# Optimization experiments

Hardware: AMD Instinct MI355X
Metric: run time of the kernel (lower is better)

## Reference

```python
import jax, jax.numpy as jnp
import numpy as np

H, D = 16, 64            # total_num_heads, head_dim
E = H * D                # embed_dim = 1024
NUM_BUCKETS, MAX_DIST = 32, 128
SCALING = D ** -0.5


def _rel_buckets(seq_len):
    # WavLM bidirectional relative position buckets (static, computed in numpy)
    ctx = np.arange(seq_len)[:, None]
    mem = np.arange(seq_len)[None, :]
    rel = mem - ctx                                  # [s, s]
    nb = NUM_BUCKETS // 2
    buckets = (rel > 0).astype(np.int64) * nb
    rp = np.abs(rel)
    max_exact = nb // 2
    is_small = rp < max_exact
    large = max_exact + (
        np.log(np.maximum(rp, 1) / max_exact) / np.log(MAX_DIST / max_exact) * (nb - max_exact)
    ).astype(np.int64)
    large = np.minimum(large, nb - 1)
    buckets = buckets + np.where(is_small, rp, large)
    return jnp.asarray(buckets)


def setup_inputs() -> dict:
    key = jax.random.key(0)
    ks = jax.random.split(key, 12)
    s = 0.02
    x = jax.random.normal(ks[0], (8, 1024, E), jnp.float32)
    Wq = jax.random.normal(ks[1], (E, H * D), jnp.float32) * s
    bq = jnp.zeros((H * D,), jnp.float32)
    Wk = jax.random.normal(ks[2], (E, H * D), jnp.float32) * s
    bk = jnp.zeros((H * D,), jnp.float32)
    Wv = jax.random.normal(ks[3], (E, H * D), jnp.float32) * s
    bv = jnp.zeros((H * D,), jnp.float32)
    Wo = jax.random.normal(ks[4], (H * D, E), jnp.float32) * s
    bo = jnp.zeros((E,), jnp.float32)
    rel_embed = jax.random.normal(ks[5], (NUM_BUCKETS, H), jnp.float32) * s
    gru_w = jax.random.normal(ks[6], (D, 8), jnp.float32) * s
    gru_b = jnp.zeros((8,), jnp.float32)
    gru_const = jnp.ones((1, H, 1, 1), jnp.float32)
    return {"x": x, "Wq": Wq, "bq": bq, "Wk": Wk, "bk": bk, "Wv": Wv, "bv": bv,
            "Wo": Wo, "bo": bo, "rel_embed": rel_embed,
            "gru_w": gru_w, "gru_b": gru_b, "gru_const": gru_const}


def reference(x, Wq, bq, Wk, bk, Wv, bv, Wo, bo, rel_embed, gru_w, gru_b, gru_const):
    b, s, e = x.shape
    # relative position bias: [H, s, s]
    buckets = _rel_buckets(s)
    pos_bias = jnp.transpose(rel_embed[buckets], (2, 0, 1))
    # gated relative position (gru_rel_pos)
    qlayer = x.reshape(b, s, H, D).transpose(0, 2, 1, 3)            # [b,H,s,D]
    g = jnp.einsum('bhsd,de->bhse', qlayer, gru_w) + gru_b          # [b,H,s,8]
    g = jax.nn.sigmoid(g.reshape(b, H, s, 2, 4).sum(-1))           # [b,H,s,2]
    gate_a, gate_b = g[..., :1], g[..., 1:]                         # [b,H,s,1]
    gate = gate_a * (gate_b * gru_const - 1.0) + 2.0                # [b,H,s,1]
    bias = gate * pos_bias[None]                                    # [b,H,s,s]
    # projections -> [b,H,s,D]
    q = (x @ Wq + bq).reshape(b, s, H, D).transpose(0, 2, 1, 3)
    k = (x @ Wk + bk).reshape(b, s, H, D).transpose(0, 2, 1, 3)
    v = (x @ Wv + bv).reshape(b, s, H, D).transpose(0, 2, 1, 3)
    scores = SCALING * jnp.einsum('bhqd,bhkd->bhqk', q, k) + bias
    w = jax.nn.softmax(scores, axis=-1)   # includes stable max-subtract
    out = jnp.einsum('bhqk,bhkd->bhqd', w, v)
    out = out.transpose(0, 2, 1, 3).reshape(b, s, H * D)
    return out @ Wo + bo
```

## Files before the change

kernel.cpp:

```cpp
#include <hip/hip_runtime.h>
#include <hip/hip_bf16.h>
#include <math.h>


typedef __attribute__((ext_vector_type(8))) short short8;
typedef __attribute__((ext_vector_type(4))) float f32x4;

#define LDSP(p) ((__attribute__((address_space(3))) void*)(p))
#define GLBP(p) ((const __attribute__((address_space(1))) void*)(p))

__device__ __forceinline__ void async_ld16(const void* src, void* dst) {
  __builtin_amdgcn_global_load_lds(GLBP(src), LDSP(dst), 16, 0, 0);
}
__device__ __forceinline__ unsigned short f2bf(float f) {
  __hip_bfloat16 h = __float2bfloat16(f);
  return __builtin_bit_cast(unsigned short, h);
}
#if __has_builtin(__builtin_amdgcn_exp2f)
#define EXP2(x) __builtin_amdgcn_exp2f(x)
#else
#define EXP2(x) exp2f(x)
#endif

__global__ __launch_bounds__(256) void prep_all(
    const float* __restrict__ x, const float* __restrict__ gw,
    const float* __restrict__ gb, const float* __restrict__ gcst,
    const float* __restrict__ W0, const float* __restrict__ W1,
    const float* __restrict__ W2, const float* __restrict__ W3,
    const float* __restrict__ rel_embed,
    unsigned short* __restrict__ xb, float* __restrict__ gate_ws,
    unsigned short* __restrict__ Wt_all, float* __restrict__ btab) {
  __shared__ __align__(16) float tile[64][68];
  const int bid = blockIdx.x, t = threadIdx.x;
  if (bid < 8192) {
    float* xr = &tile[0][0];
    const float4 v = *(const float4*)&x[(size_t)bid * 1024 + t * 4];
    *(float4*)&xr[t * 4] = v;
    ushort4 o;
    o.x = f2bf(v.x); o.y = f2bf(v.y); o.z = f2bf(v.z); o.w = f2bf(v.w);
    *(ushort4*)&xb[(size_t)bid * 1024 + t * 4] = o;
    __syncthreads();
    const int h = t >> 4, i = t & 15;
    float pa = 0.f, pb = 0.f;
    #pragma unroll
    for (int j = 0; j < 4; ++j) {
      const int d = i * 4 + j;
      const float xv = xr[h * 64 + d];
      const float* wr = &gw[d * 8];
      pa += xv * (wr[0] + wr[1] + wr[2] + wr[3]);
      pb += xv * (wr[4] + wr[5] + wr[6] + wr[7]);
    }
    #pragma unroll
    for (int msk = 1; msk <= 8; msk <<= 1) {
      pa += __shfl_xor(pa, msk);
      pb += __shfl_xor(pb, msk);
    }
    if (i == 0) {
      const float ba = gb[0] + gb[1] + gb[2] + gb[3];
      const float bb = gb[4] + gb[5] + gb[6] + gb[7];
      const float ga  = 1.f / (1.f + __expf(-(pa + ba)));
      const float gbv = 1.f / (1.f + __expf(-(pb + bb)));
      const float gv  = ga * (gbv * gcst[h] - 1.f) + 2.f;
      const int b = bid >> 10, s = bid & 1023;
      gate_ws[(b * 16 + h) * 1024 + s] = gv;
    }
  } else if (bid < 9216) {
    const int zz = bid - 8192;
    const int z = zz >> 8;
    const float* W = (z == 0) ? W0 : (z == 1) ? W1 : (z == 2) ? W2 : W3;
    unsigned short* Wt = Wt_all + (size_t)z * 1048576;
    const int n0 = (zz & 15) * 64, k0 = ((zz >> 4) & 15) * 64;
    const int c = (t & 15) * 4, r = t >> 4;
    #pragma unroll
    for (int i = 0; i < 4; ++i)
      *(float4*)&tile[r + i * 16][c] =
          *(const float4*)&W[(size_t)(k0 + r + i * 16) * 1024 + n0 + c];
    __syncthreads();
    #pragma unroll
    for (int i = 0; i < 4; ++i) {
      const int n = r + i * 16;
      ushort4 o;
      o.x = f2bf(tile[c + 0][n]); o.y = f2bf(tile[c + 1][n]);
      o.z = f2bf(tile[c + 2][n]); o.w = f2bf(tile[c + 3][n]);
      *(ushort4*)&Wt[(size_t)(n0 + n) * 1024 + k0 + c] = o;
    }
  } else {
    const int idx = (bid - 9216) * 256 + t;
    if (idx < 2047) {
      const int rel = idx - 1023;
      int bucket = (rel > 0) ? 16 : 0;
      const int rp = rel < 0 ? -rel : rel;
      if (rp < 8) {
        bucket += rp;
      } else {
        const double lv = log((double)rp / 8.0) / log(16.0) * 8.0;
        int large = 8 + (int)lv;
        bucket += (large < 15) ? large : 15;
      }
      #pragma unroll
      for (int h = 0; h < 16; ++h)
        btab[h * 2048 + idx] = rel_embed[bucket * 16 + h];
    }
  }
}

template <int SWAP>
__device__ __forceinline__ void gemm_core(
    const unsigned short* __restrict__ A, const unsigned short* __restrict__ Bt,
    unsigned short* As, unsigned short* Bs, const int m0, const int n0,
    f32x4 acc[4][4]) {
  const int t = threadIdx.x, w = t >> 6, l = t & 63;
  const int lr = l & 15, lg = l >> 4;
  const int wr = w >> 1, wc = w & 1;

  const unsigned short* asrc[4];
  const unsigned short* bsrc[4];
  unsigned short* adst[4];
  unsigned short* bdst[4];
  #pragma unroll
  for (int i = 0; i < 4; ++i) {
    const int p = (w * 4 + i) * 64 + l, r = p >> 3, c = p & 7;
    const int cs = c ^ (r & 7);
    asrc[i] = A + (size_t)(m0 + r) * 1024 + cs * 8;
    bsrc[i] = Bt + (size_t)(n0 + r) * 1024 + cs * 8;
    adst[i] = &As[(w * 4 + i) * 512];
    bdst[i] = &Bs[(w * 4 + i) * 512];
  }

  int offA[2][4], offB[2][4];
  #pragma unroll
  for (int ks = 0; ks < 2; ++ks)
    #pragma unroll
    for (int mt = 0; mt < 4; ++mt) {
      offA[ks][mt] = (wr * 64 + mt * 16 + lr) * 64 + ((ks * 4 + lg) ^ (lr & 7)) * 8;
      offB[ks][mt] = (wc * 64 + mt * 16 + lr) * 64 + ((ks * 4 + lg) ^ (lr & 7)) * 8;
    }

  for (int k0 = 0; k0 < 16; ++k0) {
    #pragma unroll
    for (int i = 0; i < 4; ++i) {
      async_ld16(asrc[i], adst[i]);
      async_ld16(bsrc[i], bdst[i]);
      asrc[i] += 64;
      bsrc[i] += 64;
    }
    __syncthreads();
    #pragma unroll
    for (int ks = 0; ks < 2; ++ks) {
      short8 af[4], bf[4];
      #pragma unroll
      for (int mt = 0; mt < 4; ++mt) af[mt] = *(const short8*)&As[offA[ks][mt]];
      #pragma unroll
      for (int nt = 0; nt < 4; ++nt) bf[nt] = *(const short8*)&Bs[offB[ks][nt]];
      #pragma unroll
      for (int mt = 0; mt < 4; ++mt)
        #pragma unroll
        for (int nt = 0; nt < 4; ++nt)
          acc[mt][nt] = SWAP
              ? __builtin_amdgcn_mfma_f32_16x16x32_bf16(bf[nt], af[mt], acc[mt][nt], 0, 0, 0)
              : __builtin_amdgcn_mfma_f32_16x16x32_bf16(af[mt], bf[nt], acc[mt][nt], 0, 0, 0);
    }
    __syncthreads();
  }
}

__global__ __launch_bounds__(256) void gemm_qkv(
    const unsigned short* __restrict__ A, const unsigned short* __restrict__ wt_all,
    const float* __restrict__ bq, const float* __restrict__ bk,
    const float* __restrict__ bv, unsigned short* __restrict__ q_ws,
    unsigned short* __restrict__ k_ws, unsigned short* __restrict__ vt_ws) {
  __shared__ __align__(16) unsigned short As[128 * 64];
  __shared__ __align__(16) unsigned short Bs[128 * 64];
  const int which = blockIdx.y >> 3;
  const int m0 = blockIdx.x * 128, n0 = (blockIdx.y & 7) * 128;
  const unsigned short* Bt = wt_all + (size_t)which * 1048576;

  const int t = threadIdx.x, w = t >> 6, l = t & 63;
  const int lr = l & 15, lg = l >> 4;
  const int wr = w >> 1, wc = w & 1;
  const int mbase = m0 + wr * 64, nbase = n0 + wc * 64;

  f32x4 acc[4][4];
  #pragma unroll
  for (int mt = 0; mt < 4; ++mt)
    #pragma unroll
    for (int nt = 0; nt < 4; ++nt) acc[mt][nt] = (f32x4){0.f, 0.f, 0.f, 0.f};

  if (which == 2) {
    gemm_core<0>(A, Bt, As, Bs, m0, n0, acc);
    #pragma unroll
    for (int mt = 0; mt < 4; ++mt) {
      const int m4 = mbase + mt * 16 + lg * 4;
      const int b = m4 >> 10, s = m4 & 1023;
      #pragma unroll
      for (int nt = 0; nt < 4; ++nt) {
        const int n = nbase + nt * 16 + lr, h = n >> 6, d = n & 63;
        const float bvv = bv[n];
        ushort4 o;
        o.x = f2bf(acc[mt][nt][0] + bvv);
        o.y = f2bf(acc[mt][nt][1] + bvv);
        o.z = f2bf(acc[mt][nt][2] + bvv);
        o.w = f2bf(acc[mt][nt][3] + bvv);
        *(ushort4*)&vt_ws[(size_t)(b * 16 + h) * 65536 + (size_t)d * 1024 + s] = o;
      }
    }
  } else {
    gemm_core<1>(A, Bt, As, Bs, m0, n0, acc);
    unsigned short* dst = (which == 0) ? q_ws : k_ws;
    const float* bias = (which == 0) ? bq : bk;
    const float scale = (which == 0) ? 0.18033688011f : 1.0f;
    #pragma unroll
    for (int nt = 0; nt < 4; ++nt) {
      const int n4 = nbase + nt * 16 + lg * 4;
      const int h = n4 >> 6, d = n4 & 63;
      const float4 b4 = *(const float4*)&bias[n4];
      #pragma unroll
      for (int mt = 0; mt < 4; ++mt) {
        const int m = mbase + mt * 16 + lr;
        const int b = m >> 10, s = m & 1023;
        ushort4 o;
        o.x = f2bf((acc[mt][nt][0] + b4.x) * scale);
        o.y = f2bf((acc[mt][nt][1] + b4.y) * scale);
        o.z = f2bf((acc[mt][nt][2] + b4.z) * scale);
        o.w = f2bf((acc[mt][nt][3] + b4.w) * scale);
        *(ushort4*)&dst[(size_t)(b * 16 + h) * 65536 + s * 64 + d] = o;
      }
    }
  }
}

__global__ __launch_bounds__(256) void gemm_out(
    const unsigned short* __restrict__ A, const unsigned short* __restrict__ Bt,
    const float* __restrict__ bias, float* __restrict__ C) {
  __shared__ __align__(16) unsigned short As[128 * 64];
  __shared__ __align__(16) unsigned short Bs[128 * 64];
  const int m0 = blockIdx.x * 128, n0 = blockIdx.y * 128;
  f32x4 acc[4][4];
  #pragma unroll
  for (int mt = 0; mt < 4; ++mt)
    #pragma unroll
    for (int nt = 0; nt < 4; ++nt) acc[mt][nt] = (f32x4){0.f, 0.f, 0.f, 0.f};
  gemm_core<1>(A, Bt, As, Bs, m0, n0, acc);

  const int t = threadIdx.x, w = t >> 6, l = t & 63;
  const int lr = l & 15, lg = l >> 4;
  const int wr = w >> 1, wc = w & 1;
  const int mbase = m0 + wr * 64, nbase = n0 + wc * 64;
  #pragma unroll
  for (int nt = 0; nt < 4; ++nt) {
    const int n4 = nbase + nt * 16 + lg * 4;
    const float4 b4 = *(const float4*)&bias[n4];
    #pragma unroll
    for (int mt = 0; mt < 4; ++mt) {
      const int m = mbase + mt * 16 + lr;
      float4 o;
      o.x = acc[mt][nt][0] + b4.x;
      o.y = acc[mt][nt][1] + b4.y;
      o.z = acc[mt][nt][2] + b4.z;
      o.w = acc[mt][nt][3] + b4.w;
      *(float4*)&C[(size_t)m * 1024 + n4] = o;
    }
  }
}

__global__ __launch_bounds__(512) void attn_mfma(
    const unsigned short* __restrict__ q_ws, const unsigned short* __restrict__ k_ws,
    const unsigned short* __restrict__ vt_ws, const float* __restrict__ gate_ws,
    const float* __restrict__ btab, unsigned short* __restrict__ ctx) {
  __shared__ __align__(16) unsigned short Ks[2][64 * 64];
  __shared__ __align__(16) unsigned short Vts[64 * 64];
  __shared__ __align__(16) unsigned short Ps[8 * 1024];
  __shared__ __align__(16) float biasl[1216];
  __shared__ float gates[128];
  __shared__ float scl[128];

  const int t = threadIdx.x, w = t >> 6, l = t & 63;
  const int lr = l & 15, lg = l >> 4;
  const int bh = blockIdx.x, h = bh & 15, b = bh >> 4;
  const int q0 = blockIdx.y * 128;
  const size_t hb = (size_t)bh * 65536;

  short8 qf[2];
  #pragma unroll
  for (int ks = 0; ks < 2; ++ks)
    qf[ks] = *(const short8*)(q_ws + hb + (size_t)(q0 + w * 16 + lr) * 64 +
                              (ks * 4 + lg) * 8);

  {
    const int p = t, r = p >> 3, c = p & 7;
    const int cs = c ^ (r & 7);
    async_ld16(k_ws + hb + (size_t)r * 64 + cs * 8, &Ks[0][w * 512]);
  }
  {
    const float* bt = btab + h * 2048 + (896 - q0);
    const int u = t * 4;
    if (u < 1216) *(float4*)&biasl[u] = *(const float4*)&bt[u];
  }
  if (t < 128) gates[t] = gate_ws[bh * 1024 + q0 + t];
  asm volatile("s_waitcnt vmcnt(0) lgkmcnt(0)" ::: "memory");
  __builtin_amdgcn_s_barrier();
  __builtin_amdgcn_sched_barrier(0);

  int pwoff[4], proff[2], offF[2][4];
  #pragma unroll
  for (int nt = 0; nt < 4; ++nt)
    pwoff[nt] = w * 2048 + ((lr * 128 + nt * 32 + lg * 8) ^ ((lr & 7) << 4));
  #pragma unroll
  for (int ks = 0; ks < 2; ++ks) {
    proff[ks] = w * 2048 + ((lr * 128 + ks * 64 + lg * 16) ^ ((lr & 7) << 4));
    #pragma unroll
    for (int nt = 0; nt < 4; ++nt)
      offF[ks][nt] = (nt * 16 + lr) * 64 + ((ks * 4 + lg) ^ (lr & 7)) * 8;
  }

  float mcur = -1e30f, lsum = 0.f;
  f32x4 acc_o[4];
  #pragma unroll
  for (int dt = 0; dt < 4; ++dt) acc_o[dt] = (f32x4){0.f, 0.f, 0.f, 0.f};
  const float gtl = gates[w * 16 + lr] * 1.44269504f;
  const int ub = 127 - w * 16 - lr;
  char* Pb = (char*)Ps;

  int pcur = 0;
  for (int kt = 0; kt < 16; ++kt) {
    {
      const int p = t, r = p >> 3, c = p & 7;
      const int cs = c ^ (r & 7);
      async_ld16(vt_ws + hb + (size_t)r * 1024 + kt * 64 + cs * 8, &Vts[w * 512]);
      if (kt < 15)
        async_ld16(k_ws + hb + (size_t)(kt + 1) * 4096 + (size_t)r * 64 + cs * 8,
                   &Ks[pcur ^ 1][w * 512]);
    }

    const int bb = kt * 64 + ub + lg * 4;
    f32x4 accs[4];
    #pragma unroll
    for (int nt = 0; nt < 4; ++nt) {
      accs[nt][0] = gtl * biasl[bb + nt * 16 + 0];
      accs[nt][1] = gtl * biasl[bb + nt * 16 + 1];
      accs[nt][2] = gtl * biasl[bb + nt * 16 + 2];
      accs[nt][3] = gtl * biasl[bb + nt * 16 + 3];
    }

    __builtin_amdgcn_s_setprio(1);
    #pragma unroll
    for (int ks = 0; ks < 2; ++ks) {
      #pragma unroll
      for (int nt = 0; nt < 4; ++nt) {
        const short8 kf = *(const short8*)&Ks[pcur][offF[ks][nt]];
        accs[nt] = __builtin_amdgcn_mfma_f32_16x16x32_bf16(kf, qf[ks], accs[nt], 0, 0, 0);
      }
    }
    __builtin_amdgcn_s_setprio(0);

    float tm = -1e30f;
    #pragma unroll
    for (int nt = 0; nt < 4; ++nt)
      tm = fmaxf(fmaxf(tm, fmaxf(accs[nt][0], accs[nt][1])),
                 fmaxf(accs[nt][2], accs[nt][3]));
    tm = fmaxf(tm, __shfl_xor(tm, 16));
    tm = fmaxf(tm, __shfl_xor(tm, 32));

    const int skip = __all(tm <= mcur + 11.5f);
    float sc = 1.0f;
    if (!skip) {
      const float mn = fmaxf(mcur, tm);
      sc = EXP2(mcur - mn);
      mcur = mn;
      if (lg == 0) scl[w * 16 + lr] = sc;
    }

    float ps = 0.f;
    #pragma unroll
    for (int nt = 0; nt < 4; ++nt) {
      const float p0 = EXP2(accs[nt][0] - mcur);
      const float p1 = EXP2(accs[nt][1] - mcur);
      const float p2 = EXP2(accs[nt][2] - mcur);
      const float p3 = EXP2(accs[nt][3] - mcur);
      ps += (p0 + p1) + (p2 + p3);
      short4 pk;
      pk.x = (short)f2bf(p0); pk.y = (short)f2bf(p1);
      pk.z = (short)f2bf(p2); pk.w = (short)f2bf(p3);
      *(short4*)(Pb + pwoff[nt]) = pk;
    }
    lsum = skip ? (lsum + ps) : (lsum * sc + ps);

    if (kt < 15) {
      asm volatile("s_waitcnt vmcnt(1) lgkmcnt(0)" ::: "memory");
    } else {
      asm volatile("s_waitcnt vmcnt(0) lgkmcnt(0)" ::: "memory");
    }
    __builtin_amdgcn_s_barrier();
    __builtin_amdgcn_sched_barrier(0);

    if (!skip) {
      const float s0 = scl[w * 16 + lg * 4 + 0];
      const float s1 = scl[w * 16 + lg * 4 + 1];
      const float s2 = scl[w * 16 + lg * 4 + 2];
      const float s3 = scl[w * 16 + lg * 4 + 3];
      #pragma unroll
      for (int dt = 0; dt < 4; ++dt) {
        acc_o[dt][0] *= s0; acc_o[dt][1] *= s1;
        acc_o[dt][2] *= s2; acc_o[dt][3] *= s3;
      }
    }

    __builtin_amdgcn_s_setprio(1);
    #pragma unroll
    for (int ks = 0; ks < 2; ++ks) {
      const short8 pf = *(const short8*)(Pb + proff[ks]);
      #pragma unroll
      for (int dt = 0; dt < 4; ++dt) {
        const short8 vf = *(const short8*)&Vts[offF[ks][dt]];
        acc_o[dt] = __builtin_amdgcn_mfma_f32_16x16x32_bf16(pf, vf, acc_o[dt], 0, 0, 0);
      }
    }
    __builtin_amdgcn_s_setprio(0);

    asm volatile("s_waitcnt vmcnt(0)" ::: "memory");
    __builtin_amdgcn_s_barrier();
    __builtin_amdgcn_sched_barrier(0);
    pcur ^= 1;
  }

  lsum += __shfl_xor(lsum, 16);
  lsum += __shfl_xor(lsum, 32);
  if (lg == 0) scl[w * 16 + lr] = 1.0f / lsum;
  asm volatile("s_waitcnt lgkmcnt(0)" ::: "memory");
  __builtin_amdgcn_s_barrier();
  float inv[4];
  #pragma unroll
  for (int i = 0; i < 4; ++i) inv[i] = scl[w * 16 + lg * 4 + i];
  #pragma unroll
  for (int i = 0; i < 4; ++i) {
    const int q = q0 + w * 16 + lg * 4 + i;
    const size_t rowoff = ((size_t)(b * 1024 + q) * 16 + h) * 64;
    #pragma unroll
    for (int dt = 0; dt < 4; ++dt)
      ctx[rowoff + dt * 16 + lr] = f2bf(acc_o[dt][i] * inv[i]);
  }
}

extern "C" void kernel_launch(void* const* d_in, const int* in_sizes, int n_in,
                              void* d_out, int out_size, void* d_ws, size_t ws_size,
                              hipStream_t stream) {
  const float* x    = (const float*)d_in[0];
  const float* Wq   = (const float*)d_in[1];
  const float* bq   = (const float*)d_in[2];
  const float* Wk   = (const float*)d_in[3];
  const float* bk   = (const float*)d_in[4];
  const float* Wv   = (const float*)d_in[5];
  const float* bv   = (const float*)d_in[6];
  const float* Wo   = (const float*)d_in[7];
  const float* bo   = (const float*)d_in[8];
  const float* rel  = (const float*)d_in[9];
  const float* gw   = (const float*)d_in[10];
  const float* gb   = (const float*)d_in[11];
  const float* gcst = (const float*)d_in[12];
  float* out = (float*)d_out;

  char* ws = (char*)d_ws;
  unsigned short* x_bf   = (unsigned short*)(ws);
  unsigned short* wt_all = (unsigned short*)(ws + 16777216);
  unsigned short* q_ws   = (unsigned short*)(ws + 25165824);
  unsigned short* k_ws   = (unsigned short*)(ws + 41943040);
  unsigned short* vt_ws  = (unsigned short*)(ws + 58720256);
  unsigned short* ctx    = (unsigned short*)(ws + 75497472);
  float* gate = (float*)(ws + 92274688);
  float* btab = (float*)(ws + 92798976);

  prep_all <<<dim3(9224),   256, 0, stream>>>(x, gw, gb, gcst, Wq, Wk, Wv, Wo,
                                              rel, x_bf, gate, wt_all, btab);
  gemm_qkv <<<dim3(64, 24), 256, 0, stream>>>(x_bf, wt_all, bq, bk, bv,
                                              q_ws, k_ws, vt_ws);
  attn_mfma<<<dim3(128, 8), 512, 0, stream>>>(q_ws, k_ws, vt_ws, gate, btab, ctx);
  gemm_out <<<dim3(64, 8),  256, 0, stream>>>(ctx, wt_all + 3 * 1048576, bo, out);
}
```

Baseline: 286.2 us.

## Drop K double-buffering in attention, trim barriers, add gemm_qkv occupancy hint

The attention kernel now uses a single K buffer. K and V tiles are loaded at the top of each iteration and waited on right away, instead of prefetching the next K tile. This frees 8 KB of LDS per block, so more blocks may fit per CU. The barrier between writing P and reading it is removed, as is the final barrier before reading the normaliser; both rely on P and scl being per-wave regions. Gates are read straight from global memory. gemm_qkv also gets a min-blocks-per-CU hint of 5. The cost is that global load latency for K is no longer hidden behind compute within a block.

```diff
diff --git a/kernel.cpp b/kernel.cpp
--- a/kernel.cpp
+++ b/kernel.cpp
@@ -164,7 +164,7 @@
   }
 }
 
-__global__ __launch_bounds__(256) void gemm_qkv(
+__global__ __launch_bounds__(256, 5) void gemm_qkv(
     const unsigned short* __restrict__ A, const unsigned short* __restrict__ wt_all,
     const float* __restrict__ bq, const float* __restrict__ bk,
     const float* __restrict__ bv, unsigned short* __restrict__ q_ws,
@@ -267,11 +267,10 @@
     const unsigned short* __restrict__ q_ws, const unsigned short* __restrict__ k_ws,
     const unsigned short* __restrict__ vt_ws, const float* __restrict__ gate_ws,
     const float* __restrict__ btab, unsigned short* __restrict__ ctx) {
-  __shared__ __align__(16) unsigned short Ks[2][64 * 64];
+  __shared__ __align__(16) unsigned short Ks[64 * 64];
   __shared__ __align__(16) unsigned short Vts[64 * 64];
   __shared__ __align__(16) unsigned short Ps[8 * 1024];
   __shared__ __align__(16) float biasl[1216];
-  __shared__ float gates[128];
   __shared__ float scl[128];
 
   const int t = threadIdx.x, w = t >> 6, l = t & 63;
@@ -287,19 +286,12 @@
                               (ks * 4 + lg) * 8);
 
   {
-    const int p = t, r = p >> 3, c = p & 7;
-    const int cs = c ^ (r & 7);
-    async_ld16(k_ws + hb + (size_t)r * 64 + cs * 8, &Ks[0][w * 512]);
-  }
-  {
     const float* bt = btab + h * 2048 + (896 - q0);
     const int u = t * 4;
     if (u < 1216) *(float4*)&biasl[u] = *(const float4*)&bt[u];
   }
-  if (t < 128) gates[t] = gate_ws[bh * 1024 + q0 + t];
-  asm volatile("s_waitcnt vmcnt(0) lgkmcnt(0)" ::: "memory");
-  __builtin_amdgcn_s_barrier();
-  __builtin_amdgcn_sched_barrier(0);
+  const float gtl = gate_ws[bh * 1024 + q0 + w * 16 + lr] * 1.44269504f;
+  __syncthreads();
 
   int pwoff[4], proff[2], offF[2][4];
   #pragma unroll
@@ -313,24 +305,22 @@
       offF[ks][nt] = (nt * 16 + lr) * 64 + ((ks * 4 + lg) ^ (lr & 7)) * 8;
   }
 
+  const int sr = t >> 3, scz = (t & 7) ^ (sr & 7);
+  const unsigned short* ksrc0 = k_ws + hb + (size_t)sr * 64 + scz * 8;
+  const unsigned short* vsrc0 = vt_ws + hb + (size_t)sr * 1024 + scz * 8;
+  unsigned short* kdst = &Ks[w * 512];
+  unsigned short* vdst = &Vts[w * 512];
+
   float mcur = -1e30f, lsum = 0.f;
   f32x4 acc_o[4];
   #pragma unroll
   for (int dt = 0; dt < 4; ++dt) acc_o[dt] = (f32x4){0.f, 0.f, 0.f, 0.f};
-  const float gtl = gates[w * 16 + lr] * 1.44269504f;
   const int ub = 127 - w * 16 - lr;
   char* Pb = (char*)Ps;
 
-  int pcur = 0;
   for (int kt = 0; kt < 16; ++kt) {
-    {
-      const int p = t, r = p >> 3, c = p & 7;
-      const int cs = c ^ (r & 7);
-      async_ld16(vt_ws + hb + (size_t)r * 1024 + kt * 64 + cs * 8, &Vts[w * 512]);
-      if (kt < 15)
-        async_ld16(k_ws + hb + (size_t)(kt + 1) * 4096 + (size_t)r * 64 + cs * 8,
-                   &Ks[pcur ^ 1][w * 512]);
-    }
+    async_ld16(ksrc0 + kt * 4096, kdst);
+    async_ld16(vsrc0 + kt * 64, vdst);
 
     const int bb = kt * 64 + ub + lg * 4;
     f32x4 accs[4];
@@ -342,12 +332,16 @@
       accs[nt][3] = gtl * biasl[bb + nt * 16 + 3];
     }
 
+    asm volatile("s_waitcnt vmcnt(0) lgkmcnt(0)" ::: "memory");
+    __builtin_amdgcn_s_barrier();
+    __builtin_amdgcn_sched_barrier(0);
+
     __builtin_amdgcn_s_setprio(1);
     #pragma unroll
     for (int ks = 0; ks < 2; ++ks) {
       #pragma unroll
       for (int nt = 0; nt < 4; ++nt) {
-        const short8 kf = *(const short8*)&Ks[pcur][offF[ks][nt]];
+        const short8 kf = *(const short8*)&Ks[offF[ks][nt]];
         accs[nt] = __builtin_amdgcn_mfma_f32_16x16x32_bf16(kf, qf[ks], accs[nt], 0, 0, 0);
       }
     }
@@ -385,12 +379,7 @@
     }
     lsum = skip ? (lsum + ps) : (lsum * sc + ps);
 
-    if (kt < 15) {
-      asm volatile("s_waitcnt vmcnt(1) lgkmcnt(0)" ::: "memory");
-    } else {
-      asm volatile("s_waitcnt vmcnt(0) lgkmcnt(0)" ::: "memory");
-    }
-    __builtin_amdgcn_s_barrier();
+    asm volatile("s_waitcnt lgkmcnt(0)" ::: "memory");
     __builtin_amdgcn_sched_barrier(0);
 
     if (!skip) {
@@ -417,17 +406,16 @@
     }
     __builtin_amdgcn_s_setprio(0);
 
-    asm volatile("s_waitcnt vmcnt(0)" ::: "memory");
+    asm volatile("s_waitcnt lgkmcnt(0)" ::: "memory");
     __builtin_amdgcn_s_barrier();
     __builtin_amdgcn_sched_barrier(0);
-    pcur ^= 1;
   }
 
   lsum += __shfl_xor(lsum, 16);
   lsum += __shfl_xor(lsum, 32);
   if (lg == 0) scl[w * 16 + lr] = 1.0f / lsum;
   asm volatile("s_waitcnt lgkmcnt(0)" ::: "memory");
-  __builtin_amdgcn_s_barrier();
+  __builtin_amdgcn_sched_barrier(0);
   float inv[4];
   #pragma unroll
   for (int i = 0; i < 4; ++i) inv[i] = scl[w * 16 + lg * 4 + i];
```

Result: slower. 391.0 us (+36.6%).
